# Kernel tuning notes

Hardware: AMD Instinct MI355X
Metric: run time of the kernel (lower is better)

The kernel has to match this reference:

```python
import jax, jax.numpy as jnp
import numpy as np

THETA = jnp.array([1.0, -0.5, 0.25, -0.125, 0.0625], dtype=jnp.float32)
N_NODES = 100000
N_EDGES = 1600000
D_FEAT = 32


def setup_inputs() -> dict:
    key = jax.random.key(0)
    k1, k2, k3 = jax.random.split(key, 3)
    feat = jax.random.normal(k1, (N_NODES, D_FEAT), dtype=jnp.float32)
    src = jax.random.randint(k2, (N_EDGES,), 0, N_NODES, dtype=jnp.int64)
    dst = jax.random.randint(k3, (N_EDGES,), 0, N_NODES, dtype=jnp.int64)
    return {"feat": feat, "src": src, "dst": dst}


def reference(feat, src, dst):
    n = feat.shape[0]
    # in-degree per node (edges counted by destination), clamped to >= 1
    deg = jax.ops.segment_sum(jnp.ones(src.shape[0], dtype=feat.dtype), dst, num_segments=n)
    d_invsqrt = jnp.maximum(deg, 1.0) ** -0.5  # [N]
    d_invsqrt = d_invsqrt[:, None]             # [N, 1]

    def unn_laplacian(f):
        # f - D^-1/2 A D^-1/2 f, via gather-from-src, scatter-sum-to-dst
        scaled = f * d_invsqrt                                   # [N, d]
        agg = jax.ops.segment_sum(scaled[src], dst, num_segments=n)  # [N, d]
        return f - agg * d_invsqrt

    h = THETA[0] * feat
    f = feat
    for k in range(1, THETA.shape[0]):
        f = unn_laplacian(f)
        h = h + THETA[k] * f
    return h
```

## Files before the change

### kernel.cpp

```cpp
#include <hip/hip_runtime.h>
#include <hip/hip_fp16.h>

#define D 32
#define BSHIFT 8
#define BNODES 256
#define NB_MAX 512
#define CHUNK 4096
#define CTHREADS 512

union H8 {
    float4 f4;
    __half2 h2[4];
};

__global__ void scatter_bucket(const int* __restrict__ src, const int* __restrict__ dst,
                               int* __restrict__ bcursor, unsigned int* __restrict__ staged,
                               int n_edges, int cap) {
    __shared__ int cnt[NB_MAX];
    __shared__ int sbase[NB_MAX];
    __shared__ int gbase[NB_MAX];
    __shared__ unsigned int stg[CHUNK];
    __shared__ unsigned short stgb[CHUNK];
    int tid = threadIdx.x;
    for (int j = tid; j < NB_MAX; j += CTHREADS) cnt[j] = 0;
    __syncthreads();
    int base = blockIdx.x * CHUNK;
    const int EPT = CHUNK / CTHREADS;
    int b8[EPT], r8[EPT], s8[EPT], d8[EPT];
    #pragma unroll
    for (int k = 0; k < EPT; ++k) {
        int i = base + k * CTHREADS + tid;
        if (i < n_edges) {
            int dv = dst[i];
            s8[k] = src[i];
            d8[k] = dv & (BNODES - 1);
            b8[k] = dv >> BSHIFT;
            r8[k] = atomicAdd(&cnt[b8[k]], 1);
        } else {
            b8[k] = -1;
        }
    }
    __syncthreads();
    int v = cnt[tid];
    sbase[tid] = v;
    __syncthreads();
    for (int off = 1; off < NB_MAX; off <<= 1) {
        int t = (tid >= off) ? sbase[tid - off] : 0;
        __syncthreads();
        sbase[tid] += t;
        __syncthreads();
    }
    int excl = sbase[tid] - v;
    __syncthreads();
    sbase[tid] = excl;
    gbase[tid] = v ? (tid * cap + atomicAdd(&bcursor[tid], v)) : 0;
    __syncthreads();
    #pragma unroll
    for (int k = 0; k < EPT; ++k) {
        if (b8[k] >= 0) {
            int p = sbase[b8[k]] + r8[k];
            stg[p] = ((unsigned)s8[k] << BSHIFT) | (unsigned)d8[k];
            stgb[p] = (unsigned short)b8[k];
        }
    }
    __syncthreads();
    int valid = n_edges - base;
    if (valid > CHUNK) valid = CHUNK;
    for (int j = tid; j < valid; j += CTHREADS) {
        int b = stgb[j];
        int idx = gbase[b] + (j - sbase[b]);
        if (idx < (b + 1) * cap)
            staged[idx] = stg[j];
    }
}

__global__ void bucket_finalize(const int* __restrict__ bcursor, const unsigned int* __restrict__ staged,
                                int cap, int* __restrict__ csr, float4* __restrict__ meta,
                                const float* __restrict__ feat, __half* __restrict__ s0,
                                int n_nodes) {
    __shared__ int cnt[BNODES];
    __shared__ int scn[BNODES];
    __shared__ int cursor[BNODES];
    __shared__ float ldinv[BNODES];
    int tid = threadIdx.x;
    int b = blockIdx.x;
    int node0 = b << BSHIFT;
    int nn = n_nodes - node0;
    if (nn > BNODES) nn = BNODES;
    int base = b * cap;
    int m = bcursor[b];
    if (m > cap) m = cap;
    if (tid < BNODES) cnt[tid] = 0;
    __syncthreads();
    for (int j = tid; j < m; j += CTHREADS)
        atomicAdd(&cnt[staged[base + j] & (BNODES - 1)], 1);
    __syncthreads();
    if (tid < BNODES) scn[tid] = cnt[tid];
    __syncthreads();
    for (int off = 1; off < BNODES; off <<= 1) {
        int t = 0;
        if (tid < BNODES && tid >= off) t = scn[tid - off];
        __syncthreads();
        if (tid < BNODES) scn[tid] += t;
        __syncthreads();
    }
    if (tid < BNODES) {
        int excl = scn[tid] - cnt[tid];
        cursor[tid] = excl;
        if (tid < nn) {
            float fd = (float)cnt[tid];
            fd = fd < 1.0f ? 1.0f : fd;
            float dn = rsqrtf(fd);
            ldinv[tid] = dn;
            float4 mt;
            mt.x = __int_as_float(base + excl);
            mt.y = __int_as_float(base + excl + cnt[tid]);
            mt.z = dn * dn;
            mt.w = sqrtf(fd);
            meta[node0 + tid] = mt;
        }
    }
    __syncthreads();
    for (int j = tid; j < m; j += CTHREADS) {
        unsigned int p = staged[base + j];
        int d = p & (BNODES - 1);
        int pos = atomicAdd(&cursor[d], 1);
        csr[base + pos] = (int)(p >> BSHIFT);
    }
    int ntask = nn * 4;
    for (int t = tid; t < ntask; t += CTHREADS) {
        int nl = t >> 2;
        int q8 = (t & 3) << 3;
        float dn = ldinv[nl];
        size_t off = ((size_t)(node0 + nl) << 5) + q8;
        float4 a = *reinterpret_cast<const float4*>(&feat[off]);
        float4 bb = *reinterpret_cast<const float4*>(&feat[off + 4]);
        H8 o;
        o.h2[0] = __floats2half2_rn(a.x * dn, a.y * dn);
        o.h2[1] = __floats2half2_rn(a.z * dn, a.w * dn);
        o.h2[2] = __floats2half2_rn(bb.x * dn, bb.y * dn);
        o.h2[3] = __floats2half2_rn(bb.z * dn, bb.w * dn);
        *reinterpret_cast<float4*>(&s0[off]) = o.f4;
    }
}

__device__ __forceinline__ void acc_row(const __half* __restrict__ s_cur, int sn, int q8,
                                        float& a0, float& a1, float& a2, float& a3,
                                        float& a4, float& a5, float& a6, float& a7) {
    H8 u;
    u.f4 = *reinterpret_cast<const float4*>(&s_cur[((size_t)sn << 5) + q8]);
    float2 p0 = __half22float2(u.h2[0]);
    float2 p1 = __half22float2(u.h2[1]);
    float2 p2 = __half22float2(u.h2[2]);
    float2 p3 = __half22float2(u.h2[3]);
    a0 += p0.x; a1 += p0.y; a2 += p1.x; a3 += p1.y;
    a4 += p2.x; a5 += p2.y; a6 += p3.x; a7 += p3.y;
}

__global__ void hop_kernel(const float4* __restrict__ meta, const int* __restrict__ csr,
                           const __half* __restrict__ s_cur, __half* __restrict__ s_next,
                           int n_nodes) {
    int t = blockIdx.x * blockDim.x + threadIdx.x;
    int node = t >> 2;
    if (node >= n_nodes) return;
    int q8 = (t & 3) << 3;
    float4 mt = meta[node];
    int e = __float_as_int(mt.x), end = __float_as_int(mt.y);
    float a0 = 0.f, a1 = 0.f, a2 = 0.f, a3 = 0.f, a4 = 0.f, a5 = 0.f, a6 = 0.f, a7 = 0.f;
    for (; e + 3 < end; e += 4) {
        int s0 = csr[e], s1 = csr[e + 1], s2 = csr[e + 2], s3 = csr[e + 3];
        acc_row(s_cur, s0, q8, a0, a1, a2, a3, a4, a5, a6, a7);
        acc_row(s_cur, s1, q8, a0, a1, a2, a3, a4, a5, a6, a7);
        acc_row(s_cur, s2, q8, a0, a1, a2, a3, a4, a5, a6, a7);
        acc_row(s_cur, s3, q8, a0, a1, a2, a3, a4, a5, a6, a7);
    }
    for (; e < end; ++e)
        acc_row(s_cur, csr[e], q8, a0, a1, a2, a3, a4, a5, a6, a7);
    size_t off = ((size_t)node << 5) + q8;
    float dn2 = mt.z;
    H8 sc;
    sc.f4 = *reinterpret_cast<const float4*>(&s_cur[off]);
    float2 c0 = __half22float2(sc.h2[0]);
    float2 c1 = __half22float2(sc.h2[1]);
    float2 c2 = __half22float2(sc.h2[2]);
    float2 c3 = __half22float2(sc.h2[3]);
    H8 so;
    so.h2[0] = __floats2half2_rn(c0.x - a0 * dn2, c0.y - a1 * dn2);
    so.h2[1] = __floats2half2_rn(c1.x - a2 * dn2, c1.y - a3 * dn2);
    so.h2[2] = __floats2half2_rn(c2.x - a4 * dn2, c2.y - a5 * dn2);
    so.h2[3] = __floats2half2_rn(c3.x - a6 * dn2, c3.y - a7 * dn2);
    *reinterpret_cast<float4*>(&s_next[off]) = so.f4;
}

__global__ void hop_last_kernel(const float4* __restrict__ meta, const int* __restrict__ csr,
                                const __half* __restrict__ s1, const __half* __restrict__ s2,
                                const __half* __restrict__ s3, const float* __restrict__ feat,
                                float* __restrict__ h, int n_nodes) {
    int t = blockIdx.x * blockDim.x + threadIdx.x;
    int node = t >> 2;
    if (node >= n_nodes) return;
    int q8 = (t & 3) << 3;
    float4 mt = meta[node];
    int e = __float_as_int(mt.x), end = __float_as_int(mt.y);
    float a0 = 0.f, a1 = 0.f, a2 = 0.f, a3 = 0.f, a4 = 0.f, a5 = 0.f, a6 = 0.f, a7 = 0.f;
    for (; e + 3 < end; e += 4) {
        int t0 = csr[e], t1 = csr[e + 1], t2 = csr[e + 2], t3 = csr[e + 3];
        acc_row(s3, t0, q8, a0, a1, a2, a3, a4, a5, a6, a7);
        acc_row(s3, t1, q8, a0, a1, a2, a3, a4, a5, a6, a7);
        acc_row(s3, t2, q8, a0, a1, a2, a3, a4, a5, a6, a7);
        acc_row(s3, t3, q8, a0, a1, a2, a3, a4, a5, a6, a7);
    }
    for (; e < end; ++e)
        acc_row(s3, csr[e], q8, a0, a1, a2, a3, a4, a5, a6, a7);
    size_t off = ((size_t)node << 5) + q8;
    float dn2 = mt.z;
    float ds = mt.w;
    H8 u1, u2, u3;
    u1.f4 = *reinterpret_cast<const float4*>(&s1[off]);
    u2.f4 = *reinterpret_cast<const float4*>(&s2[off]);
    u3.f4 = *reinterpret_cast<const float4*>(&s3[off]);
    float4 fa = *reinterpret_cast<const float4*>(&feat[off]);
    float4 fb = *reinterpret_cast<const float4*>(&feat[off + 4]);
    const float th1 = -0.5f, th2 = 0.25f, th3 = -0.125f, th4 = 0.0625f;
    float r[8] = {fa.x, fa.y, fa.z, fa.w, fb.x, fb.y, fb.z, fb.w};
    float aa[8] = {a0, a1, a2, a3, a4, a5, a6, a7};
    #pragma unroll
    for (int j = 0; j < 4; ++j) {
        float2 p1 = __half22float2(u1.h2[j]);
        float2 p2 = __half22float2(u2.h2[j]);
        float2 p3 = __half22float2(u3.h2[j]);
        float s4x = p3.x - aa[2 * j] * dn2;
        float s4y = p3.y - aa[2 * j + 1] * dn2;
        float mx = fmaf(th1, p1.x, fmaf(th2, p2.x, fmaf(th3, p3.x, th4 * s4x)));
        float my = fmaf(th1, p1.y, fmaf(th2, p2.y, fmaf(th3, p3.y, th4 * s4y)));
        r[2 * j]     = fmaf(ds, mx, r[2 * j]);
        r[2 * j + 1] = fmaf(ds, my, r[2 * j + 1]);
    }
    float4 o0 = {r[0], r[1], r[2], r[3]};
    float4 o1 = {r[4], r[5], r[6], r[7]};
    *reinterpret_cast<float4*>(&h[off]) = o0;
    *reinterpret_cast<float4*>(&h[off + 4]) = o1;
}

extern "C" void kernel_launch(void* const* d_in, const int* in_sizes, int n_in,
                              void* d_out, int out_size, void* d_ws, size_t ws_size,
                              hipStream_t stream) {
    const float* feat = (const float*)d_in[0];
    const int*   src  = (const int*)d_in[1];
    const int*   dst  = (const int*)d_in[2];
    float* h = (float*)d_out;

    int n_nodes = in_sizes[0] / D;
    int n_edges = in_sizes[1];
    long long total_nf = (long long)n_nodes * D;
    int nb = (n_nodes + BNODES - 1) >> BSHIFT;
    int cap = (int)(((2LL * n_edges / nb) + 1023) & ~1023LL);

    char* w = (char*)d_ws;
    auto alloc = [&](size_t bytes) {
        char* p = w;
        w += (bytes + 15) & ~(size_t)15;
        return (void*)p;
    };
    int*          bcursor = (int*)alloc(NB_MAX * 4);
    float4*       meta    = (float4*)alloc((size_t)n_nodes * 16);
    unsigned int* staged  = (unsigned int*)alloc((size_t)nb * cap * 4);
    int*          csr     = (int*)alloc((size_t)nb * cap * 4);
    __half*       s[4];
    for (int k = 0; k < 4; ++k) s[k] = (__half*)alloc((size_t)total_nf * 2);

    hipMemsetAsync(bcursor, 0, NB_MAX * sizeof(int), stream);
    int eblocks = (n_edges + CHUNK - 1) / CHUNK;
    scatter_bucket<<<eblocks, CTHREADS, 0, stream>>>(src, dst, bcursor, staged, n_edges, cap);
    bucket_finalize<<<nb, CTHREADS, 0, stream>>>(bcursor, staged, cap, csr, meta,
                                                 feat, s[0], n_nodes);

    int hop_threads = n_nodes * 4;
    int hop_blocks = (hop_threads + 255) / 256;
    for (int k = 1; k < 4; ++k)
        hop_kernel<<<hop_blocks, 256, 0, stream>>>(meta, csr, s[k - 1], s[k], n_nodes);
    hop_last_kernel<<<hop_blocks, 256, 0, stream>>>(meta, csr,
                                                    s[1], s[2], s[3], feat, h, n_nodes);
}
```

Before: 134.0 us.

## Fuse four hop kernels into one cooperative kernel with grid syncs

Replaces the three hop launches and the final hop launch with a single cooperative kernel. Each thread handles two node-quarter slots and keeps its self values and the running theta-weighted accumulator in registers across hops, separated by grid-wide syncs. This removes launch gaps and the re-reading of s1/s2/s3 and self rows in the last hop. In exchange it adds grid-barrier cost and relies on all 782 blocks being co-resident (checked against a hardcoded 256 CUs), falling back to the old kernels otherwise.

Result: no change. 133.8 us (-0.2%).

```diff
diff --git a/kernel.cpp b/kernel.cpp
--- a/kernel.cpp
+++ b/kernel.cpp
@@ -1,5 +1,8 @@
 #include <hip/hip_runtime.h>
 #include <hip/hip_fp16.h>
+#include <hip/hip_cooperative_groups.h>
+
+namespace cg = cooperative_groups;
 
 #define D 32
 #define BSHIFT 8
@@ -7,6 +10,8 @@
 #define NB_MAX 512
 #define CHUNK 4096
 #define CTHREADS 512
+#define HTHREADS 256
+#define NUM_CUS 256
 
 union H8 {
     float4 f4;
@@ -144,18 +149,17 @@
     }
 }
 
-__device__ __forceinline__ void acc_row(const __half* __restrict__ s_cur, int sn, int q8,
-                                        float& a0, float& a1, float& a2, float& a3,
-                                        float& a4, float& a5, float& a6, float& a7) {
+__device__ __forceinline__ void add_row(const __half* __restrict__ tab, int sn, int q8, float* a) {
     H8 u;
-    u.f4 = *reinterpret_cast<const float4*>(&s_cur[((size_t)sn << 5) + q8]);
+    u.f4 = *reinterpret_cast<const float4*>(&tab[((size_t)sn << 5) + q8]);
     float2 p0 = __half22float2(u.h2[0]);
     float2 p1 = __half22float2(u.h2[1]);
     float2 p2 = __half22float2(u.h2[2]);
     float2 p3 = __half22float2(u.h2[3]);
-    a0 += p0.x; a1 += p0.y; a2 += p1.x; a3 += p1.y;
-    a4 += p2.x; a5 += p2.y; a6 += p3.x; a7 += p3.y;
-}
+    a[0] += p0.x; a[1] += p0.y; a[2] += p1.x; a[3] += p1.y;
+    a[4] += p2.x; a[5] += p2.y; a[6] += p3.x; a[7] += p3.y;
+}
+
 
 __global__ void hop_kernel(const float4* __restrict__ meta, const int* __restrict__ csr,
                            const __half* __restrict__ s_cur, __half* __restrict__ s_next,
@@ -166,16 +170,16 @@
     int q8 = (t & 3) << 3;
     float4 mt = meta[node];
     int e = __float_as_int(mt.x), end = __float_as_int(mt.y);
-    float a0 = 0.f, a1 = 0.f, a2 = 0.f, a3 = 0.f, a4 = 0.f, a5 = 0.f, a6 = 0.f, a7 = 0.f;
+    float a[8] = {0.f, 0.f, 0.f, 0.f, 0.f, 0.f, 0.f, 0.f};
     for (; e + 3 < end; e += 4) {
-        int s0 = csr[e], s1 = csr[e + 1], s2 = csr[e + 2], s3 = csr[e + 3];
-        acc_row(s_cur, s0, q8, a0, a1, a2, a3, a4, a5, a6, a7);
-        acc_row(s_cur, s1, q8, a0, a1, a2, a3, a4, a5, a6, a7);
-        acc_row(s_cur, s2, q8, a0, a1, a2, a3, a4, a5, a6, a7);
-        acc_row(s_cur, s3, q8, a0, a1, a2, a3, a4, a5, a6, a7);
+        int i0 = csr[e], i1 = csr[e + 1], i2 = csr[e + 2], i3 = csr[e + 3];
+        add_row(s_cur, i0, q8, a);
+        add_row(s_cur, i1, q8, a);
+        add_row(s_cur, i2, q8, a);
+        add_row(s_cur, i3, q8, a);
     }
     for (; e < end; ++e)
-        acc_row(s_cur, csr[e], q8, a0, a1, a2, a3, a4, a5, a6, a7);
+        add_row(s_cur, csr[e], q8, a);
     size_t off = ((size_t)node << 5) + q8;
     float dn2 = mt.z;
     H8 sc;
@@ -185,10 +189,10 @@
     float2 c2 = __half22float2(sc.h2[2]);
     float2 c3 = __half22float2(sc.h2[3]);
     H8 so;
-    so.h2[0] = __floats2half2_rn(c0.x - a0 * dn2, c0.y - a1 * dn2);
-    so.h2[1] = __floats2half2_rn(c1.x - a2 * dn2, c1.y - a3 * dn2);
-    so.h2[2] = __floats2half2_rn(c2.x - a4 * dn2, c2.y - a5 * dn2);
-    so.h2[3] = __floats2half2_rn(c3.x - a6 * dn2, c3.y - a7 * dn2);
+    so.h2[0] = __floats2half2_rn(c0.x - a[0] * dn2, c0.y - a[1] * dn2);
+    so.h2[1] = __floats2half2_rn(c1.x - a[2] * dn2, c1.y - a[3] * dn2);
+    so.h2[2] = __floats2half2_rn(c2.x - a[4] * dn2, c2.y - a[5] * dn2);
+    so.h2[3] = __floats2half2_rn(c3.x - a[6] * dn2, c3.y - a[7] * dn2);
     *reinterpret_cast<float4*>(&s_next[off]) = so.f4;
 }
 
@@ -202,16 +206,16 @@
     int q8 = (t & 3) << 3;
     float4 mt = meta[node];
     int e = __float_as_int(mt.x), end = __float_as_int(mt.y);
-    float a0 = 0.f, a1 = 0.f, a2 = 0.f, a3 = 0.f, a4 = 0.f, a5 = 0.f, a6 = 0.f, a7 = 0.f;
+    float a[8] = {0.f, 0.f, 0.f, 0.f, 0.f, 0.f, 0.f, 0.f};
     for (; e + 3 < end; e += 4) {
-        int t0 = csr[e], t1 = csr[e + 1], t2 = csr[e + 2], t3 = csr[e + 3];
-        acc_row(s3, t0, q8, a0, a1, a2, a3, a4, a5, a6, a7);
-        acc_row(s3, t1, q8, a0, a1, a2, a3, a4, a5, a6, a7);
-        acc_row(s3, t2, q8, a0, a1, a2, a3, a4, a5, a6, a7);
-        acc_row(s3, t3, q8, a0, a1, a2, a3, a4, a5, a6, a7);
+        int i0 = csr[e], i1 = csr[e + 1], i2 = csr[e + 2], i3 = csr[e + 3];
+        add_row(s3, i0, q8, a);
+        add_row(s3, i1, q8, a);
+        add_row(s3, i2, q8, a);
+        add_row(s3, i3, q8, a);
     }
     for (; e < end; ++e)
-        acc_row(s3, csr[e], q8, a0, a1, a2, a3, a4, a5, a6, a7);
+        add_row(s3, csr[e], q8, a);
     size_t off = ((size_t)node << 5) + q8;
     float dn2 = mt.z;
     float ds = mt.w;
@@ -223,14 +227,13 @@
     float4 fb = *reinterpret_cast<const float4*>(&feat[off + 4]);
     const float th1 = -0.5f, th2 = 0.25f, th3 = -0.125f, th4 = 0.0625f;
     float r[8] = {fa.x, fa.y, fa.z, fa.w, fb.x, fb.y, fb.z, fb.w};
-    float aa[8] = {a0, a1, a2, a3, a4, a5, a6, a7};
     #pragma unroll
     for (int j = 0; j < 4; ++j) {
         float2 p1 = __half22float2(u1.h2[j]);
         float2 p2 = __half22float2(u2.h2[j]);
         float2 p3 = __half22float2(u3.h2[j]);
-        float s4x = p3.x - aa[2 * j] * dn2;
-        float s4y = p3.y - aa[2 * j + 1] * dn2;
+        float s4x = p3.x - a[2 * j] * dn2;
+        float s4y = p3.y - a[2 * j + 1] * dn2;
         float mx = fmaf(th1, p1.x, fmaf(th2, p2.x, fmaf(th3, p3.x, th4 * s4x)));
         float my = fmaf(th1, p1.y, fmaf(th2, p2.y, fmaf(th3, p3.y, th4 * s4y)));
         r[2 * j]     = fmaf(ds, mx, r[2 * j]);
@@ -240,6 +243,123 @@
     float4 o1 = {r[4], r[5], r[6], r[7]};
     *reinterpret_cast<float4*>(&h[off]) = o0;
     *reinterpret_cast<float4*>(&h[off + 4]) = o1;
+}
+
+
+__device__ __forceinline__ void do_phase(int node, int q8, int e, int end, float dn2,
+                                         const int* __restrict__ csr,
+                                         const __half* __restrict__ scur,
+                                         __half* __restrict__ snext,
+                                         float* self, float* hacc, float th, int n_nodes) {
+    if (node >= n_nodes) return;
+    float a[8] = {0.f, 0.f, 0.f, 0.f, 0.f, 0.f, 0.f, 0.f};
+    for (; e + 3 < end; e += 4) {
+        int i0 = csr[e], i1 = csr[e + 1], i2 = csr[e + 2], i3 = csr[e + 3];
+        add_row(scur, i0, q8, a);
+        add_row(scur, i1, q8, a);
+        add_row(scur, i2, q8, a);
+        add_row(scur, i3, q8, a);
+    }
+    for (; e < end; ++e)
+        add_row(scur, csr[e], q8, a);
+    #pragma unroll
+    for (int i = 0; i < 8; ++i)
+        self[i] = self[i] - a[i] * dn2;
+    if (snext) {
+        H8 o;
+        o.h2[0] = __floats2half2_rn(self[0], self[1]);
+        o.h2[1] = __floats2half2_rn(self[2], self[3]);
+        o.h2[2] = __floats2half2_rn(self[4], self[5]);
+        o.h2[3] = __floats2half2_rn(self[6], self[7]);
+        *reinterpret_cast<float4*>(&snext[((size_t)node << 5) + q8]) = o.f4;
+        float2 r0 = __half22float2(o.h2[0]);
+        float2 r1 = __half22float2(o.h2[1]);
+        float2 r2 = __half22float2(o.h2[2]);
+        float2 r3 = __half22float2(o.h2[3]);
+        self[0] = r0.x; self[1] = r0.y; self[2] = r1.x; self[3] = r1.y;
+        self[4] = r2.x; self[5] = r2.y; self[6] = r3.x; self[7] = r3.y;
+    }
+    #pragma unroll
+    for (int i = 0; i < 8; ++i)
+        hacc[i] = fmaf(th, self[i], hacc[i]);
+}
+
+__global__ void __launch_bounds__(HTHREADS, 4)
+hops_fused(const float4* __restrict__ meta, const int* __restrict__ csr,
+           const __half* __restrict__ s0, __half* __restrict__ s1,
+           __half* __restrict__ s2, __half* __restrict__ s3,
+           const float* __restrict__ feat, float* __restrict__ h, int n_nodes) {
+    cg::grid_group grid = cg::this_grid();
+    int tid = blockIdx.x * blockDim.x + threadIdx.x;
+    int stride = gridDim.x * blockDim.x;
+    int qA = tid, qB = tid + stride;
+    int nodeA = qA >> 2, nodeB = qB >> 2;
+    int q8A = (qA & 3) << 3, q8B = (qB & 3) << 3;
+
+    int eA0 = 0, eA1 = 0, eB0 = 0, eB1 = 0;
+    float dn2A = 0.f, dsA = 0.f, dn2B = 0.f, dsB = 0.f;
+    float selfA[8] = {0}, haccA[8] = {0}, selfB[8] = {0}, haccB[8] = {0};
+
+    if (nodeA < n_nodes) {
+        float4 mt = meta[nodeA];
+        eA0 = __float_as_int(mt.x); eA1 = __float_as_int(mt.y);
+        dn2A = mt.z; dsA = mt.w;
+        H8 u;
+        u.f4 = *reinterpret_cast<const float4*>(&s0[((size_t)nodeA << 5) + q8A]);
+        float2 r0 = __half22float2(u.h2[0]), r1 = __half22float2(u.h2[1]);
+        float2 r2 = __half22float2(u.h2[2]), r3 = __half22float2(u.h2[3]);
+        selfA[0] = r0.x; selfA[1] = r0.y; selfA[2] = r1.x; selfA[3] = r1.y;
+        selfA[4] = r2.x; selfA[5] = r2.y; selfA[6] = r3.x; selfA[7] = r3.y;
+    }
+    if (nodeB < n_nodes) {
+        float4 mt = meta[nodeB];
+        eB0 = __float_as_int(mt.x); eB1 = __float_as_int(mt.y);
+        dn2B = mt.z; dsB = mt.w;
+        H8 u;
+        u.f4 = *reinterpret_cast<const float4*>(&s0[((size_t)nodeB << 5) + q8B]);
+        float2 r0 = __half22float2(u.h2[0]), r1 = __half22float2(u.h2[1]);
+        float2 r2 = __half22float2(u.h2[2]), r3 = __half22float2(u.h2[3]);
+        selfB[0] = r0.x; selfB[1] = r0.y; selfB[2] = r1.x; selfB[3] = r1.y;
+        selfB[4] = r2.x; selfB[5] = r2.y; selfB[6] = r3.x; selfB[7] = r3.y;
+    }
+
+    do_phase(nodeA, q8A, eA0, eA1, dn2A, csr, s0, s1, selfA, haccA, -0.5f, n_nodes);
+    do_phase(nodeB, q8B, eB0, eB1, dn2B, csr, s0, s1, selfB, haccB, -0.5f, n_nodes);
+    __threadfence();
+    grid.sync();
+    do_phase(nodeA, q8A, eA0, eA1, dn2A, csr, s1, s2, selfA, haccA, 0.25f, n_nodes);
+    do_phase(nodeB, q8B, eB0, eB1, dn2B, csr, s1, s2, selfB, haccB, 0.25f, n_nodes);
+    __threadfence();
+    grid.sync();
+    do_phase(nodeA, q8A, eA0, eA1, dn2A, csr, s2, s3, selfA, haccA, -0.125f, n_nodes);
+    do_phase(nodeB, q8B, eB0, eB1, dn2B, csr, s2, s3, selfB, haccB, -0.125f, n_nodes);
+    __threadfence();
+    grid.sync();
+    do_phase(nodeA, q8A, eA0, eA1, dn2A, csr, s3, nullptr, selfA, haccA, 0.0625f, n_nodes);
+    do_phase(nodeB, q8B, eB0, eB1, dn2B, csr, s3, nullptr, selfB, haccB, 0.0625f, n_nodes);
+
+    if (nodeA < n_nodes) {
+        size_t off = ((size_t)nodeA << 5) + q8A;
+        float4 fa = *reinterpret_cast<const float4*>(&feat[off]);
+        float4 fb = *reinterpret_cast<const float4*>(&feat[off + 4]);
+        float4 o0 = {fmaf(dsA, haccA[0], fa.x), fmaf(dsA, haccA[1], fa.y),
+                     fmaf(dsA, haccA[2], fa.z), fmaf(dsA, haccA[3], fa.w)};
+        float4 o1 = {fmaf(dsA, haccA[4], fb.x), fmaf(dsA, haccA[5], fb.y),
+                     fmaf(dsA, haccA[6], fb.z), fmaf(dsA, haccA[7], fb.w)};
+        *reinterpret_cast<float4*>(&h[off]) = o0;
+        *reinterpret_cast<float4*>(&h[off + 4]) = o1;
+    }
+    if (nodeB < n_nodes) {
+        size_t off = ((size_t)nodeB << 5) + q8B;
+        float4 fa = *reinterpret_cast<const float4*>(&feat[off]);
+        float4 fb = *reinterpret_cast<const float4*>(&feat[off + 4]);
+        float4 o0 = {fmaf(dsB, haccB[0], fa.x), fmaf(dsB, haccB[1], fa.y),
+                     fmaf(dsB, haccB[2], fa.z), fmaf(dsB, haccB[3], fa.w)};
+        float4 o1 = {fmaf(dsB, haccB[4], fb.x), fmaf(dsB, haccB[5], fb.y),
+                     fmaf(dsB, haccB[6], fb.z), fmaf(dsB, haccB[7], fb.w)};
+        *reinterpret_cast<float4*>(&h[off]) = o0;
+        *reinterpret_cast<float4*>(&h[off + 4]) = o1;
+    }
 }
 
 extern "C" void kernel_launch(void* const* d_in, const int* in_sizes, int n_in,
@@ -275,8 +395,22 @@
     bucket_finalize<<<nb, CTHREADS, 0, stream>>>(bcursor, staged, cap, csr, meta,
                                                  feat, s[0], n_nodes);
 
-    int hop_threads = n_nodes * 4;
-    int hop_blocks = (hop_threads + 255) / 256;
+    int n_quads = n_nodes * 4;
+    int hblocks = (n_quads + 2 * HTHREADS - 1) / (2 * HTHREADS);
+    int maxActive = 0;
+    hipError_t qerr = hipOccupancyMaxActiveBlocksPerMultiprocessor(
+        &maxActive, hops_fused, HTHREADS, 0);
+    bool coop_ok = (qerr == hipSuccess) && ((long long)maxActive * NUM_CUS >= hblocks);
+    if (coop_ok) {
+        const __half* s0c = s[0];
+        void* args[] = {(void*)&meta, (void*)&csr, (void*)&s0c, (void*)&s[1],
+                        (void*)&s[2], (void*)&s[3], (void*)&feat, (void*)&h, (void*)&n_nodes};
+        hipError_t lerr = hipLaunchCooperativeKernel((const void*)hops_fused,
+                                                     dim3(hblocks), dim3(HTHREADS),
+                                                     args, 0, stream);
+        if (lerr == hipSuccess) return;
+    }
+    int hop_blocks = (n_quads + 255) / 256;
     for (int k = 1; k < 4; ++k)
         hop_kernel<<<hop_blocks, 256, 0, stream>>>(meta, csr, s[k - 1], s[k], n_nodes);
     hop_last_kernel<<<hop_blocks, 256, 0, stream>>>(meta, csr,
```
